# Performance work log

Measured on AMD Instinct MI355X. Metric: run time of the kernel, lower is better.

Reference implementation:

```python
import jax, jax.numpy as jnp
import numpy as np

D_MODEL = 256
NHEAD = 8
HEAD_DIM = D_MODEL // NHEAD
LN_EPS = 1e-5


def _layernorm(x, g, b):
    mu = jnp.mean(x, axis=-1, keepdims=True)
    var = jnp.mean(jnp.square(x - mu), axis=-1, keepdims=True)
    return (x - mu) * jax.lax.rsqrt(var + LN_EPS) * g + b


def setup_inputs() -> dict:
    key = jax.random.key(0)
    ks = jax.random.split(key, 12)
    N, L, S, K = 2, 4800, 4800, 64
    x = jax.random.normal(ks[0], (N, L, D_MODEL), dtype=jnp.float32)
    source = jax.random.normal(ks[1], (N, S, D_MODEL), dtype=jnp.float32)
    # precomputed epipolar-band key indices per query ([N, L, K])
    epipolar_idx = jax.random.randint(ks[2], (N, L, K), 0, S, dtype=jnp.int32)
    w = lambda k, shape: (jax.random.normal(k, shape, dtype=jnp.float32) * 0.02)
    return {
        "x": x, "source": source, "epipolar_idx": epipolar_idx,
        "Wq": w(ks[3], (D_MODEL, D_MODEL)),
        "Wk": w(ks[4], (D_MODEL, D_MODEL)),
        "Wv": w(ks[5], (D_MODEL, D_MODEL)),
        "Wm": w(ks[6], (D_MODEL, D_MODEL)),
        "W1": w(ks[7], (2 * D_MODEL, 2 * D_MODEL)),
        "W2": w(ks[8], (2 * D_MODEL, D_MODEL)),
        "g1": jnp.ones((D_MODEL,), jnp.float32),
        "b1": jnp.zeros((D_MODEL,), jnp.float32),
        "g2": jnp.ones((D_MODEL,), jnp.float32),
        "b2": jnp.zeros((D_MODEL,), jnp.float32),
    }


def reference(x, source, epipolar_idx, Wq, Wk, Wv, Wm, W1, W2, g1, b1, g2, b2):
    N, L, _ = x.shape
    q = (x @ Wq).reshape(N, L, NHEAD, HEAD_DIM)            # [N,L,H,D]
    k = (source @ Wk).reshape(N, -1, NHEAD, HEAD_DIM)      # [N,S,H,D]
    v = (source @ Wv).reshape(N, -1, NHEAD, HEAD_DIM)
    # one-to-many gather: each query attends only to its epipolar-band keys
    gather = jax.vmap(lambda t, i: t[i])                   # [N,L,K,H,D]
    kg = gather(k, epipolar_idx)
    vg = gather(v, epipolar_idx)
    scale = 1.0 / jnp.sqrt(jnp.asarray(HEAD_DIM, x.dtype))
    scores = jnp.einsum('nlhd,nlkhd->nlhk', q, kg) * scale
    attn = jax.nn.softmax(scores, axis=-1)
    msg = jnp.einsum('nlhk,nlkhd->nlhd', attn, vg).reshape(N, L, D_MODEL)
    msg = _layernorm(msg @ Wm, g1, b1)
    h = jnp.concatenate([x, msg], axis=-1) @ W1            # [N,L,2C]
    h = jax.nn.relu(h) @ W2                                # [N,L,C]
    return x + _layernorm(h, g2, b2)
```

## Files before the change

kernel.cpp:

```cpp
#include <hip/hip_runtime.h>
#include <hip/hip_bf16.h>

#define D_MODEL 256
#define LQ 4800
#define NB 2
#define MROWS (NB * LQ)
#define LN_EPS 1e-5f

typedef unsigned int u32;
typedef unsigned short u16;
typedef __attribute__((ext_vector_type(8))) short bf16x8;
typedef __attribute__((ext_vector_type(4))) float f32x4;
typedef __attribute__((ext_vector_type(2))) _Float16 f16x2;

__device__ __forceinline__ u16 f2bf(float f) {
    __hip_bfloat16 h = __float2bfloat16(f);
    return *reinterpret_cast<u16*>(&h);
}

__device__ __forceinline__ float dot2f16(u32 a, u32 b, float c) {
#if __has_builtin(__builtin_amdgcn_fdot2)
    return __builtin_amdgcn_fdot2(__builtin_bit_cast(f16x2, a),
                                  __builtin_bit_cast(f16x2, b), c, false);
#else
    f16x2 av = __builtin_bit_cast(f16x2, a), bv = __builtin_bit_cast(f16x2, b);
    c = fmaf((float)av.x, (float)bv.x, c);
    return fmaf((float)av.y, (float)bv.y, c);
#endif
}
__device__ __forceinline__ u32 pk_fma16(u32 a, u32 b, u32 c) {
    u32 d;
    asm("v_pk_fma_f16 %0, %1, %2, %3" : "=v"(d) : "v"(a), "v"(b), "v"(c));
    return d;
}
__device__ __forceinline__ u32 pk_add16(u32 a, u32 b) {
    u32 d;
    asm("v_pk_add_f16 %0, %1, %2" : "=v"(d) : "v"(a), "v"(b));
    return d;
}
__device__ __forceinline__ u32 pkrtz(float a, float b) {
    return __builtin_bit_cast(u32, __builtin_amdgcn_cvt_pkrtz(a, b));
}
__device__ __forceinline__ void gload_lds(const u16* src, u16* dst) {
    __builtin_amdgcn_global_load_lds(
        (const __attribute__((address_space(1))) u32*)src,
        (__attribute__((address_space(3))) u32*)dst, 16, 0, 0);
}

__global__ __launch_bounds__(256) void prep_kernel(
    const float* __restrict__ x, const float* __restrict__ source,
    const float* __restrict__ Wq, const float* __restrict__ Wk,
    const float* __restrict__ Wv, const float* __restrict__ Wm,
    const float* __restrict__ W1, const float* __restrict__ W2,
    u16* __restrict__ xb, u16* __restrict__ sb,
    u16* __restrict__ Wqkvt, u16* __restrict__ Wmt,
    u16* __restrict__ W1t, u16* __restrict__ W2t)
{
    __shared__ float tile[16][17];
    const int t = threadIdx.x;
    int bid = blockIdx.x;

    if (bid < 4800) {
        const float* src = bid < 2400 ? x : source;
        u16* dst = bid < 2400 ? xb : sb;
        int b = bid < 2400 ? bid : bid - 2400;
        int i = (b * 256 + t) * 4;
        float4 v = *reinterpret_cast<const float4*>(src + i);
        ushort4 o; o.x = f2bf(v.x); o.y = f2bf(v.y); o.z = f2bf(v.z); o.w = f2bf(v.w);
        *reinterpret_cast<ushort4*>(dst + i) = o;
        return;
    }
    int sub = bid - 4800;
    const float* W; u16* Wt; int Nd, ldt, rowoff;
    if      (sub < 256)  { W = Wq; Wt = Wqkvt; Nd = 256; ldt = 256; rowoff = 0;   }
    else if (sub < 512)  { W = Wk; Wt = Wqkvt; Nd = 256; ldt = 256; rowoff = 256; sub -= 256; }
    else if (sub < 768)  { W = Wv; Wt = Wqkvt; Nd = 256; ldt = 256; rowoff = 512; sub -= 512; }
    else if (sub < 1024) { W = Wm; Wt = Wmt;   Nd = 256; ldt = 256; rowoff = 0;   sub -= 768; }
    else if (sub < 2048) { W = W1; Wt = W1t;   Nd = 512; ldt = 512; rowoff = 0;   sub -= 1024; }
    else                 { W = W2; Wt = W2t;   Nd = 256; ldt = 512; rowoff = 0;   sub -= 2048; }
    int ntiles = Nd >> 4;
    int tn = sub % ntiles, tk = sub / ntiles;
    int tx = t & 15, ty = t >> 4;
    tile[ty][tx] = W[(size_t)(tk * 16 + ty) * Nd + tn * 16 + tx];
    __syncthreads();
    Wt[(size_t)(rowoff + tn * 16 + ty) * ldt + tk * 16 + tx] = f2bf(tile[tx][ty]);
}

template<int BM, int BN>
__global__ __launch_bounds__(256) void gemm_mfma_kernel(
    const u16* __restrict__ A0, int lda0,
    const u16* __restrict__ A1, int lda1, int splitK, int nsel,
    const u16* __restrict__ Bt, int ldb,
    void* __restrict__ Cout,
    int M, int N, int K, int flags)
{
    __shared__ __align__(16) u16 As[BM * 32];
    __shared__ __align__(16) u16 Bs[BN * 32];

    constexpr int WM = BM / 2, WN = BN / 2;
    constexpr int FI = WM / 16, FJ = WN / 16;

    const int t  = threadIdx.x;
    const int l  = t & 63;
    const int w  = t >> 6;
    const int m0 = blockIdx.y * BM;
    const int n0 = blockIdx.x * BN;
    const int wr = w >> 1, wc = w & 1;

    if (nsel && n0 >= nsel) { A0 = A1; lda0 = lda1; }

    const int srow = l >> 2;
    const int sch  = (l & 3) ^ (srow & 3);

    f32x4 acc[FI][FJ];
#pragma unroll
    for (int i = 0; i < FI; ++i)
#pragma unroll
        for (int j = 0; j < FJ; ++j) acc[i][j] = (f32x4){0.f, 0.f, 0.f, 0.f};

    for (int k0 = 0; k0 < K; k0 += 32) {
        const u16* Ap; int kk, lda;
        if (splitK && k0 >= splitK) { Ap = A1; kk = k0 - splitK; lda = lda1; }
        else                        { Ap = A0; kk = k0;          lda = lda0; }

        if (BM >= 64) {
#pragma unroll
            for (int g = 0; g < BM / 64; ++g) {
                int grp = w * (BM / 64) + g;
                int row = grp * 16 + srow;
                gload_lds(Ap + (size_t)(m0 + row) * lda + kk + sch * 8, As + grp * 512);
            }
        } else if (w < BM / 16) {
            int row = w * 16 + srow;
            gload_lds(Ap + (size_t)(m0 + row) * lda + kk + sch * 8, As + w * 512);
        }
#pragma unroll
        for (int g = 0; g < BN / 64; ++g) {
            int grp = w * (BN / 64) + g;
            int row = grp * 16 + srow;
            gload_lds(Bt + (size_t)(n0 + row) * ldb + k0 + sch * 8, Bs + grp * 512);
        }
        __syncthreads();

        const int r  = l & 15;
        const int ch = l >> 4;
        bf16x8 af[FI], bfr[FJ];
#pragma unroll
        for (int i = 0; i < FI; ++i) {
            int ar = wr * WM + i * 16 + r;
            af[i] = *(const bf16x8*)((const char*)As + ar * 64 + ((ch ^ (r & 3)) * 16));
        }
#pragma unroll
        for (int j = 0; j < FJ; ++j) {
            int br = wc * WN + j * 16 + r;
            bfr[j] = *(const bf16x8*)((const char*)Bs + br * 64 + ((ch ^ (r & 3)) * 16));
        }
#pragma unroll
        for (int i = 0; i < FI; ++i)
#pragma unroll
            for (int j = 0; j < FJ; ++j)
                acc[i][j] = __builtin_amdgcn_mfma_f32_16x16x32_bf16(af[i], bfr[j], acc[i][j], 0, 0, 0);
        __syncthreads();
    }

    const int r  = l & 15;
    const int q4 = l >> 4;
#pragma unroll
    for (int i = 0; i < FI; ++i)
#pragma unroll
        for (int j = 0; j < FJ; ++j) {
            int col = n0 + wc * WN + j * 16 + r;
#pragma unroll
            for (int reg = 0; reg < 4; ++reg) {
                int row = m0 + wr * WM + i * 16 + q4 * 4 + reg;
                float vv = acc[i][j][reg];
                if (flags & 1) vv = fmaxf(vv, 0.f);
                size_t off;
                int colw, Nw;
                if (flags & 4) { off = (size_t)(col >> 8) * M * 256; colw = col & 255; Nw = 256; }
                else           { off = 0; colw = col; Nw = N; }
                if (flags & 8) {
                    _Float16 hv = (_Float16)vv;
                    ((u16*)Cout)[off + (size_t)row * Nw + colw] = __builtin_bit_cast(u16, hv);
                } else if (flags & 2) {
                    ((u16*)Cout)[off + (size_t)row * Nw + colw] = f2bf(vv);
                } else {
                    ((float*)Cout)[off + (size_t)row * Nw + colw] = vv;
                }
            }
        }
}

template<int FJ>
__device__ __forceinline__ void mm_loop(
    const u16* __restrict__ A0, int lda0,
    const u16* __restrict__ A1, int lda1, int splitK,
    const u16* __restrict__ Bt, int ldb, int K, int m0,
    u16* As, u16* Bs, f32x4 (&acc)[FJ])
{
    const int t = threadIdx.x;
    const int l = t & 63, w = t >> 6;
    const int wr = w >> 1, wc = w & 1;
    const int srow = l >> 2;
    const int sch  = (l & 3) ^ (srow & 3);
    const int r = l & 15, ch = l >> 4;

#pragma unroll
    for (int j = 0; j < FJ; ++j) acc[j] = (f32x4){0.f, 0.f, 0.f, 0.f};

    for (int k0 = 0; k0 < K; k0 += 32) {
        const u16* Ap; int kk, lda;
        if (splitK && k0 >= splitK) { Ap = A1; kk = k0 - splitK; lda = lda1; }
        else                        { Ap = A0; kk = k0;          lda = lda0; }
        if (w < 2) {
            int row = w * 16 + srow;
            gload_lds(Ap + (size_t)(m0 + row) * lda + kk + sch * 8, As + w * 512);
        }
#pragma unroll
        for (int g = 0; g < FJ / 2; ++g) {
            int grp = w * (FJ / 2) + g;
            int row = grp * 16 + srow;
            gload_lds(Bt + (size_t)row * ldb + k0 + sch * 8, Bs + grp * 512);
        }
        __syncthreads();
        bf16x8 af = *(const bf16x8*)((const char*)As + (wr * 16 + r) * 64 + ((ch ^ (r & 3)) * 16));
#pragma unroll
        for (int j = 0; j < FJ; ++j) {
            int br = wc * (FJ * 16) + j * 16 + r;
            bf16x8 bf = *(const bf16x8*)((const char*)Bs + br * 64 + ((ch ^ (r & 3)) * 16));
            acc[j] = __builtin_amdgcn_mfma_f32_16x16x32_bf16(af, bf, acc[j], 0, 0, 0);
        }
        __syncthreads();
    }
}

__global__ __launch_bounds__(256) void tail_kernel(
    const u16* __restrict__ msg, const u16* __restrict__ xb,
    const float* __restrict__ x,
    const u16* __restrict__ Wmt, const u16* __restrict__ W1t,
    const u16* __restrict__ W2t,
    const float* __restrict__ g1, const float* __restrict__ b1,
    const float* __restrict__ g2, const float* __restrict__ b2,
    u16* __restrict__ msglnb, u16* __restrict__ h1b,
    float* __restrict__ out)
{
    __shared__ __align__(16) u16 As[32 * 32];
    __shared__ __align__(16) u16 Bs[512 * 32];
    __shared__ float2 red[32][2];

    const int t = threadIdx.x;
    const int l = t & 63, w = t >> 6;
    const int wr = w >> 1, wc = w & 1;
    const int m0 = blockIdx.x * 32;
    const int r = l & 15, q4 = l >> 4;

    {
        f32x4 acc[8];
        mm_loop<8>(msg, 256, nullptr, 0, 0, Wmt, 256, 256, m0, As, Bs, acc);

        float rs[4], rq[4];
#pragma unroll
        for (int reg = 0; reg < 4; ++reg) {
            float s = 0.f, sq = 0.f;
#pragma unroll
            for (int j = 0; j < 8; ++j) { float vv = acc[j][reg]; s += vv; sq += vv * vv; }
            rs[reg] = s; rq[reg] = sq;
        }
#pragma unroll
        for (int off = 1; off <= 8; off <<= 1)
#pragma unroll
            for (int reg = 0; reg < 4; ++reg) {
                rs[reg] += __shfl_xor(rs[reg], off);
                rq[reg] += __shfl_xor(rq[reg], off);
            }
        if (r == 0)
#pragma unroll
            for (int reg = 0; reg < 4; ++reg)
                red[wr * 16 + q4 * 4 + reg][wc] = make_float2(rs[reg], rq[reg]);
        __syncthreads();

#pragma unroll
        for (int reg = 0; reg < 4; ++reg) {
            int row = wr * 16 + q4 * 4 + reg;
            float2 t0 = red[row][0], t1 = red[row][1];
            float mu  = (t0.x + t1.x) * 0.00390625f;
            float var = (t0.y + t1.y) * 0.00390625f - mu * mu;
            float rstd = rsqrtf(var + LN_EPS);
#pragma unroll
            for (int j = 0; j < 8; ++j) {
                int col = wc * 128 + j * 16 + r;
                float vv = (acc[j][reg] - mu) * rstd * g1[col] + b1[col];
                msglnb[(size_t)(m0 + row) * 256 + col] = f2bf(vv);
            }
        }
    }
    __threadfence_block();
    __syncthreads();

    {
        f32x4 acc[16];
        mm_loop<16>(xb, 256, msglnb, 256, 256, W1t, 512, 512, m0, As, Bs, acc);
#pragma unroll
        for (int j = 0; j < 16; ++j) {
            int col = wc * 256 + j * 16 + r;
#pragma unroll
            for (int reg = 0; reg < 4; ++reg) {
                int row = wr * 16 + q4 * 4 + reg;
                float vv = fmaxf(acc[j][reg], 0.f);
                h1b[(size_t)(m0 + row) * 512 + col] = f2bf(vv);
            }
        }
    }
    __threadfence_block();
    __syncthreads();

    {
        f32x4 acc[8];
        mm_loop<8>(h1b, 512, nullptr, 0, 0, W2t, 512, 512, m0, As, Bs, acc);

        float rs[4], rq[4];
#pragma unroll
        for (int reg = 0; reg < 4; ++reg) {
            float s = 0.f, sq = 0.f;
#pragma unroll
            for (int j = 0; j < 8; ++j) { float vv = acc[j][reg]; s += vv; sq += vv * vv; }
            rs[reg] = s; rq[reg] = sq;
        }
#pragma unroll
        for (int off = 1; off <= 8; off <<= 1)
#pragma unroll
            for (int reg = 0; reg < 4; ++reg) {
                rs[reg] += __shfl_xor(rs[reg], off);
                rq[reg] += __shfl_xor(rq[reg], off);
            }
        __syncthreads();
        if (r == 0)
#pragma unroll
            for (int reg = 0; reg < 4; ++reg)
                red[wr * 16 + q4 * 4 + reg][wc] = make_float2(rs[reg], rq[reg]);
        __syncthreads();

#pragma unroll
        for (int reg = 0; reg < 4; ++reg) {
            int row = wr * 16 + q4 * 4 + reg;
            float2 t0 = red[row][0], t1 = red[row][1];
            float mu  = (t0.x + t1.x) * 0.00390625f;
            float var = (t0.y + t1.y) * 0.00390625f - mu * mu;
            float rstd = rsqrtf(var + LN_EPS);
#pragma unroll
            for (int j = 0; j < 8; ++j) {
                int col = wc * 128 + j * 16 + r;
                size_t oidx = (size_t)(m0 + row) * 256 + col;
                float vv = (acc[j][reg] - mu) * rstd * g2[col] + b2[col] + x[oidx];
                out[oidx] = vv;
            }
        }
    }
}

__global__ __launch_bounds__(256, 8) void attn_kernel(
    const u16* __restrict__ q, const u16* __restrict__ k,
    const u16* __restrict__ v, const int* __restrict__ idx,
    u16* __restrict__ msg)
{
    const int t  = threadIdx.x;
    const int l  = t & 63;
    const int hp = t >> 6;
    const int qi = blockIdx.x;
    const int n  = qi / LQ;
    const size_t srcbase = (size_t)n * LQ * 256;

    const int o = l >> 3;
    const int c = l & 7;

    const int* idxp = idx + (size_t)qi * 64;
    int rows[8];
#pragma unroll
    for (int i = 0; i < 8; ++i) rows[i] = idxp[i * 8 + o];

    const size_t hoff = (size_t)hp * 64 + c * 8;

    uint4 kd[8];
#pragma unroll
    for (int i = 0; i < 8; ++i)
        kd[i] = *(const uint4*)(k + srcbase + (size_t)rows[i] * 256 + hoff);
    uint4 qc = *(const uint4*)(q + (size_t)qi * 256 + hoff);

    float s[8];
#pragma unroll
    for (int i = 0; i < 8; ++i) {
        float si = 0.f;
        si = dot2f16(kd[i].x, qc.x, si);
        si = dot2f16(kd[i].y, qc.y, si);
        si = dot2f16(kd[i].z, qc.z, si);
        si = dot2f16(kd[i].w, qc.w, si);
        si += __shfl_xor(si, 1);
        si += __shfl_xor(si, 2);
        s[i] = si * 0.17677669529663687f;
    }

    uint4 vd[8];
#pragma unroll
    for (int i = 0; i < 8; ++i)
        vd[i] = *(const uint4*)(v + srcbase + (size_t)rows[i] * 256 + hoff);

    float mx = s[0];
#pragma unroll
    for (int i = 1; i < 8; ++i) mx = fmaxf(mx, s[i]);
    mx = fmaxf(mx, __shfl_xor(mx, 8));
    mx = fmaxf(mx, __shfl_xor(mx, 16));
    mx = fmaxf(mx, __shfl_xor(mx, 32));
    float p[8], sum = 0.f;
#pragma unroll
    for (int i = 0; i < 8; ++i) { p[i] = __expf(s[i] - mx); sum += p[i]; }
    sum += __shfl_xor(sum, 8);
    sum += __shfl_xor(sum, 16);
    sum += __shfl_xor(sum, 32);
    float inv = 1.f / sum;

    u32 A0 = 0, A1 = 0, A2 = 0, A3 = 0;
#pragma unroll
    for (int i = 0; i < 8; ++i) {
        float pi = p[i] * inv;
        u32 pp = pkrtz(pi, pi);
        A0 = pk_fma16(pp, vd[i].x, A0);
        A1 = pk_fma16(pp, vd[i].y, A1);
        A2 = pk_fma16(pp, vd[i].z, A2);
        A3 = pk_fma16(pp, vd[i].w, A3);
    }

    const bool ob0 = (o & 1) != 0;
    const bool ob1 = (o & 2) != 0;
    {
        u32 t0 = ob0 ? A0 : A2;
        u32 t1 = ob0 ? A1 : A3;
        t0 = __shfl_xor((int)t0, 8);
        t1 = __shfl_xor((int)t1, 8);
        A0 = pk_add16(ob0 ? A2 : A0, t0);
        A1 = pk_add16(ob0 ? A3 : A1, t1);
    }
    {
        u32 u0 = ob1 ? A0 : A1;
        u0 = __shfl_xor((int)u0, 16);
        A0 = pk_add16(ob1 ? A1 : A0, u0);
    }
    A0 = pk_add16(A0, (u32)__shfl_xor((int)A0, 32));

    if (o < 4) {
        int j = 2 * (o & 1) + ((o >> 1) & 1);
        f16x2 hv = __builtin_bit_cast(f16x2, A0);
        u32 packed = (u32)f2bf((float)hv.x) | ((u32)f2bf((float)hv.y) << 16);
        *(u32*)(msg + (size_t)qi * 256 + hp * 64 + c * 8 + j * 2) = packed;
    }
}

extern "C" void kernel_launch(void* const* d_in, const int* in_sizes, int n_in,
                              void* d_out, int out_size, void* d_ws, size_t ws_size,
                              hipStream_t stream)
{
    const float* x      = (const float*)d_in[0];
    const float* source = (const float*)d_in[1];
    const int*   eidx   = (const int*)d_in[2];
    const float* Wq     = (const float*)d_in[3];
    const float* Wk     = (const float*)d_in[4];
    const float* Wv     = (const float*)d_in[5];
    const float* Wm     = (const float*)d_in[6];
    const float* W1     = (const float*)d_in[7];
    const float* W2     = (const float*)d_in[8];
    const float* g1     = (const float*)d_in[9];
    const float* b1     = (const float*)d_in[10];
    const float* g2     = (const float*)d_in[11];
    const float* b2     = (const float*)d_in[12];
    float* out = (float*)d_out;

    char* ws = (char*)d_ws;
    const size_t SZB = (size_t)MROWS * 256 * 2;
    u16* xb     = (u16*)(ws);
    u16* sb     = (u16*)(ws + SZB);
    u16* qb     = (u16*)(ws + 2 * SZB);
    u16* kb     = (u16*)(ws + 3 * SZB);
    u16* vb     = (u16*)(ws + 4 * SZB);
    u16* msgb   = (u16*)(ws + 5 * SZB);
    u16* msglnb = (u16*)(ws + 6 * SZB);
    u16* h1b    = (u16*)(ws + 7 * SZB);
    u16* Wqkvt  = (u16*)(ws + 9 * SZB);
    u16* Wmt    = Wqkvt + 768 * 256;
    u16* W1t    = Wmt + 256 * 256;
    u16* W2t    = W1t + 512 * 512;

    dim3 blk(256);

    prep_kernel<<<dim3(7360), blk, 0, stream>>>(x, source, Wq, Wk, Wv, Wm, W1, W2,
                                                xb, sb, Wqkvt, Wmt, W1t, W2t);

    gemm_mfma_kernel<64, 128><<<dim3(6, 150), blk, 0, stream>>>(
        xb, 256, sb, 256, 0, 256, Wqkvt, 256, qb, MROWS, 768, 256, 8 | 4);

    attn_kernel<<<dim3(MROWS), blk, 0, stream>>>(qb, kb, vb, eidx, msgb);

    tail_kernel<<<dim3(300), blk, 0, stream>>>(
        msgb, xb, x, Wmt, W1t, W2t, g1, b1, g2, b2, msglnb, h1b, out);
}
```

Baseline: 100.1 us.

## Halve tail kernel row tile to 16 for more blocks; remap attention block order

The fused tail kernel (Wm GEMM+LN, W1 GEMM+ReLU, W2 GEMM+LN+residual) now processes 16 rows per block instead of 32, with each of the four waves covering a quarter of the output columns. This doubles the grid from 300 to 600 blocks so the device's compute units are better filled, at the cost of re-streaming the weight matrices twice as often per row. Separately, the attention kernel's block index is permuted so consecutive blocks map to queries spread across both batches and eight contiguous chunks, presumably to balance or localize the key/value gathers across XCDs.

```diff
diff --git a/kernel.cpp b/kernel.cpp
--- a/kernel.cpp
+++ b/kernel.cpp
@@ -192,7 +192,7 @@
 }
 
 template<int FJ>
-__device__ __forceinline__ void mm_loop(
+__device__ __forceinline__ void mm_loop16(
     const u16* __restrict__ A0, int lda0,
     const u16* __restrict__ A1, int lda1, int splitK,
     const u16* __restrict__ Bt, int ldb, int K, int m0,
@@ -200,7 +200,6 @@
 {
     const int t = threadIdx.x;
     const int l = t & 63, w = t >> 6;
-    const int wr = w >> 1, wc = w & 1;
     const int srow = l >> 2;
     const int sch  = (l & 3) ^ (srow & 3);
     const int r = l & 15, ch = l >> 4;
@@ -212,21 +211,19 @@
         const u16* Ap; int kk, lda;
         if (splitK && k0 >= splitK) { Ap = A1; kk = k0 - splitK; lda = lda1; }
         else                        { Ap = A0; kk = k0;          lda = lda0; }
-        if (w < 2) {
-            int row = w * 16 + srow;
-            gload_lds(Ap + (size_t)(m0 + row) * lda + kk + sch * 8, As + w * 512);
-        }
-#pragma unroll
-        for (int g = 0; g < FJ / 2; ++g) {
-            int grp = w * (FJ / 2) + g;
+        if (w == 0)
+            gload_lds(Ap + (size_t)(m0 + srow) * lda + kk + sch * 8, As);
+#pragma unroll
+        for (int g = 0; g < FJ; ++g) {
+            int grp = w * FJ + g;
             int row = grp * 16 + srow;
             gload_lds(Bt + (size_t)row * ldb + k0 + sch * 8, Bs + grp * 512);
         }
         __syncthreads();
-        bf16x8 af = *(const bf16x8*)((const char*)As + (wr * 16 + r) * 64 + ((ch ^ (r & 3)) * 16));
+        bf16x8 af = *(const bf16x8*)((const char*)As + r * 64 + ((ch ^ (r & 3)) * 16));
 #pragma unroll
         for (int j = 0; j < FJ; ++j) {
-            int br = wc * (FJ * 16) + j * 16 + r;
+            int br = w * (FJ * 16) + j * 16 + r;
             bf16x8 bf = *(const bf16x8*)((const char*)Bs + br * 64 + ((ch ^ (r & 3)) * 16));
             acc[j] = __builtin_amdgcn_mfma_f32_16x16x32_bf16(af, bf, acc[j], 0, 0, 0);
         }
@@ -244,26 +241,25 @@
     u16* __restrict__ msglnb, u16* __restrict__ h1b,
     float* __restrict__ out)
 {
-    __shared__ __align__(16) u16 As[32 * 32];
+    __shared__ __align__(16) u16 As[16 * 32];
     __shared__ __align__(16) u16 Bs[512 * 32];
-    __shared__ float2 red[32][2];
+    __shared__ float2 red[16][4];
 
     const int t = threadIdx.x;
     const int l = t & 63, w = t >> 6;
-    const int wr = w >> 1, wc = w & 1;
-    const int m0 = blockIdx.x * 32;
+    const int m0 = blockIdx.x * 16;
     const int r = l & 15, q4 = l >> 4;
 
     {
-        f32x4 acc[8];
-        mm_loop<8>(msg, 256, nullptr, 0, 0, Wmt, 256, 256, m0, As, Bs, acc);
+        f32x4 acc[4];
+        mm_loop16<4>(msg, 256, nullptr, 0, 0, Wmt, 256, 256, m0, As, Bs, acc);
 
         float rs[4], rq[4];
 #pragma unroll
         for (int reg = 0; reg < 4; ++reg) {
             float s = 0.f, sq = 0.f;
 #pragma unroll
-            for (int j = 0; j < 8; ++j) { float vv = acc[j][reg]; s += vv; sq += vv * vv; }
+            for (int j = 0; j < 4; ++j) { float vv = acc[j][reg]; s += vv; sq += vv * vv; }
             rs[reg] = s; rq[reg] = sq;
         }
 #pragma unroll
@@ -276,19 +272,21 @@
         if (r == 0)
 #pragma unroll
             for (int reg = 0; reg < 4; ++reg)
-                red[wr * 16 + q4 * 4 + reg][wc] = make_float2(rs[reg], rq[reg]);
+                red[q4 * 4 + reg][w] = make_float2(rs[reg], rq[reg]);
         __syncthreads();
 
 #pragma unroll
         for (int reg = 0; reg < 4; ++reg) {
-            int row = wr * 16 + q4 * 4 + reg;
-            float2 t0 = red[row][0], t1 = red[row][1];
-            float mu  = (t0.x + t1.x) * 0.00390625f;
-            float var = (t0.y + t1.y) * 0.00390625f - mu * mu;
+            int row = q4 * 4 + reg;
+            float sum = 0.f, sq = 0.f;
+#pragma unroll
+            for (int u = 0; u < 4; ++u) { sum += red[row][u].x; sq += red[row][u].y; }
+            float mu  = sum * 0.00390625f;
+            float var = sq * 0.00390625f - mu * mu;
             float rstd = rsqrtf(var + LN_EPS);
 #pragma unroll
-            for (int j = 0; j < 8; ++j) {
-                int col = wc * 128 + j * 16 + r;
+            for (int j = 0; j < 4; ++j) {
+                int col = w * 64 + j * 16 + r;
                 float vv = (acc[j][reg] - mu) * rstd * g1[col] + b1[col];
                 msglnb[(size_t)(m0 + row) * 256 + col] = f2bf(vv);
             }
@@ -298,14 +296,14 @@
     __syncthreads();
 
     {
-        f32x4 acc[16];
-        mm_loop<16>(xb, 256, msglnb, 256, 256, W1t, 512, 512, m0, As, Bs, acc);
-#pragma unroll
-        for (int j = 0; j < 16; ++j) {
-            int col = wc * 256 + j * 16 + r;
+        f32x4 acc[8];
+        mm_loop16<8>(xb, 256, msglnb, 256, 256, W1t, 512, 512, m0, As, Bs, acc);
+#pragma unroll
+        for (int j = 0; j < 8; ++j) {
+            int col = w * 128 + j * 16 + r;
 #pragma unroll
             for (int reg = 0; reg < 4; ++reg) {
-                int row = wr * 16 + q4 * 4 + reg;
+                int row = q4 * 4 + reg;
                 float vv = fmaxf(acc[j][reg], 0.f);
                 h1b[(size_t)(m0 + row) * 512 + col] = f2bf(vv);
             }
@@ -315,15 +313,15 @@
     __syncthreads();
 
     {
-        f32x4 acc[8];
-        mm_loop<8>(h1b, 512, nullptr, 0, 0, W2t, 512, 512, m0, As, Bs, acc);
+        f32x4 acc[4];
+        mm_loop16<4>(h1b, 512, nullptr, 0, 0, W2t, 512, 512, m0, As, Bs, acc);
 
         float rs[4], rq[4];
 #pragma unroll
         for (int reg = 0; reg < 4; ++reg) {
             float s = 0.f, sq = 0.f;
 #pragma unroll
-            for (int j = 0; j < 8; ++j) { float vv = acc[j][reg]; s += vv; sq += vv * vv; }
+            for (int j = 0; j < 4; ++j) { float vv = acc[j][reg]; s += vv; sq += vv * vv; }
             rs[reg] = s; rq[reg] = sq;
         }
 #pragma unroll
@@ -337,19 +335,21 @@
         if (r == 0)
 #pragma unroll
             for (int reg = 0; reg < 4; ++reg)
-                red[wr * 16 + q4 * 4 + reg][wc] = make_float2(rs[reg], rq[reg]);
+                red[q4 * 4 + reg][w] = make_float2(rs[reg], rq[reg]);
         __syncthreads();
 
 #pragma unroll
         for (int reg = 0; reg < 4; ++reg) {
-            int row = wr * 16 + q4 * 4 + reg;
-            float2 t0 = red[row][0], t1 = red[row][1];
-            float mu  = (t0.x + t1.x) * 0.00390625f;
-            float var = (t0.y + t1.y) * 0.00390625f - mu * mu;
+            int row = q4 * 4 + reg;
+            float sum = 0.f, sq = 0.f;
+#pragma unroll
+            for (int u = 0; u < 4; ++u) { sum += red[row][u].x; sq += red[row][u].y; }
+            float mu  = sum * 0.00390625f;
+            float var = sq * 0.00390625f - mu * mu;
             float rstd = rsqrtf(var + LN_EPS);
 #pragma unroll
-            for (int j = 0; j < 8; ++j) {
-                int col = wc * 128 + j * 16 + r;
+            for (int j = 0; j < 4; ++j) {
+                int col = w * 64 + j * 16 + r;
                 size_t oidx = (size_t)(m0 + row) * 256 + col;
                 float vv = (acc[j][reg] - mu) * rstd * g2[col] + b2[col] + x[oidx];
                 out[oidx] = vv;
@@ -366,7 +366,9 @@
     const int t  = threadIdx.x;
     const int l  = t & 63;
     const int hp = t >> 6;
-    const int qi = blockIdx.x;
+    const int bid = blockIdx.x;
+    const int x8 = bid & 7, jj = bid >> 3;
+    const int qi = (x8 < 4) ? (x8 * 1200 + jj) : (LQ + (x8 - 4) * 1200 + jj);
     const int n  = qi / LQ;
     const size_t srcbase = (size_t)n * LQ * 256;
 
@@ -498,6 +500,6 @@
 
     attn_kernel<<<dim3(MROWS), blk, 0, stream>>>(qb, kb, vb, eidx, msgb);
 
-    tail_kernel<<<dim3(300), blk, 0, stream>>>(
+    tail_kernel<<<dim3(600), blk, 0, stream>>>(
         msgb, xb, x, Wmt, W1t, W2t, g1, b1, g2, b2, msglnb, h1b, out);
 }
```

New measurement: 106.8 us. 1.07x slower.
